# Kernel tuning notes

Measured on AMD Instinct MI355X. Metric: run time of the kernel, lower is better.

Reference implementation:

```python
import jax, jax.numpy as jnp
import numpy as np

FP8_MAX = 448.0  # e4m3 max, from scale = max(w) / (448.0 * 6.0) in the source


def setup_inputs() -> dict:
    key = jax.random.key(0)
    k_w, k_perm, k_x, k_b = jax.random.split(key, 4)
    T, K, O = 8192, 4096, 4096  # tokens = bsz*q_len, in_features, out_features

    # --- simulate init-time reorder_quantize_w ---
    w = jax.random.normal(k_w, (O, K), dtype=jnp.float32) * 0.02
    g_scale = jnp.max(jnp.abs(w)) / (FP8_MAX * 6.0)          # global weight scale
    perm = jax.random.permutation(k_perm, K)                  # outlier reorder index
    w_r = w[:, perm] / g_scale                                # reordered, globally scaled
    scale_w = jnp.max(jnp.abs(w_r), axis=1) / FP8_MAX         # per-out-channel scale (O,)
    W = jnp.round(w_r / scale_w[:, None])                     # quantized values (stored fp32)

    # --- simulate activation quantization (same reorder applied upstream) ---
    x = jax.random.normal(k_x, (T, K), dtype=jnp.float32)
    scale_x = (jnp.max(jnp.abs(x), axis=1, keepdims=True) / FP8_MAX)  # (T,1)
    qx = jnp.round(x / scale_x)                               # quantized values (stored fp32)

    bias = jax.random.normal(k_b, (O,), dtype=jnp.float32) * 0.01
    scale = jnp.asarray([g_scale], dtype=jnp.float32)         # fused global scale (x-global * w-global)

    return {"qx": qx, "W": W, "scale_x": scale_x, "scale_w": scale_w,
            "scale": scale, "bias": bias, "bsz": 4, "q_len": 2048}


def reference(qx, W, scale_x, scale_w, scale, bias, bsz, q_len):
    # agemm.matmul: low-bit GEMM with fused per-token (scale_x), per-channel (scale_w)
    # and global (scale) dequant scales.  y[t,o] = (sum_k qx[t,k]*W[o,k]) * sx[t] * sw[o] * s
    y = jnp.einsum('tk,ok->to', qx, W)           # (T, O) accumulate
    y = y * scale_x * scale_w[None, :] * scale[0]
    y = y + bias
    return y.reshape(bsz, q_len, -1)
```

## Files before the change

kernel.cpp:

```cpp
#include <hip/hip_runtime.h>

typedef __bf16 bf16_t;
typedef __bf16 bf16x8 __attribute__((ext_vector_type(8)));
typedef __bf16 bf16x4 __attribute__((ext_vector_type(4)));
typedef float f32x4 __attribute__((ext_vector_type(4)));

constexpr int TDIM = 8192;
constexpr int KDIM = 4096;
constexpr int ODIM = 4096;

__device__ __forceinline__ void async_ld16(void* lds, const void* g) {
    __builtin_amdgcn_global_load_lds(
        (const __attribute__((address_space(1))) unsigned int*)g,
        (__attribute__((address_space(3))) unsigned int*)lds,
        16, 0, 0);
}

__global__ __launch_bounds__(256) void cvt2_kernel(const float* __restrict__ a, bf16_t* __restrict__ da,
                                                   int nblk_a,
                                                   const float* __restrict__ w, bf16_t* __restrict__ dw) {
    int b = blockIdx.x;
    const float* src;
    bf16_t* dst;
    if (b < nblk_a) { src = a; dst = da; }
    else            { src = w; dst = dw; b -= nblk_a; }
    const size_t base = (size_t)b * 2048 + threadIdx.x * 8;
    const float4 v0 = *(const float4*)(src + base);
    const float4 v1 = *(const float4*)(src + base + 4);
    bf16x8 o;
    o[0] = (bf16_t)v0.x; o[1] = (bf16_t)v0.y; o[2] = (bf16_t)v0.z; o[3] = (bf16_t)v0.w;
    o[4] = (bf16_t)v1.x; o[5] = (bf16_t)v1.y; o[6] = (bf16_t)v1.z; o[7] = (bf16_t)v1.w;
    *(bf16x8*)(dst + base) = o;
}

constexpr int BM = 256, BN = 256, BK = 64;
constexpr int NKT = KDIM / BK;
constexpr int NIT = NKT / 2;

#define BAR   __builtin_amdgcn_s_barrier()
#define SCB   __builtin_amdgcn_sched_barrier(0)
#define WLG   asm volatile("s_waitcnt lgkmcnt(0)" ::: "memory")
#define WV6   asm volatile("s_waitcnt vmcnt(6)" ::: "memory")
#define WV0   asm volatile("s_waitcnt vmcnt(0)" ::: "memory")
#define PRIO1 __builtin_amdgcn_s_setprio(1)
#define PRIO0 __builtin_amdgcn_s_setprio(0)

#define STG_A(c, kt, h) \
    async_ld16(lds_a + (c)*32768 + (h)*16384,        a_srcb + (size_t)((h)*128     )*KDIM + (kt)*64); \
    async_ld16(lds_a + (c)*32768 + (h)*16384 + 8192, a_srcb + (size_t)((h)*128 + 64)*KDIM + (kt)*64)
#define STG_B(c, kt, h) \
    async_ld16(lds_b + (c)*32768 + (h)*16384,        b_srcb + (size_t)((h)*128     )*KDIM + (kt)*64); \
    async_ld16(lds_b + (c)*32768 + (h)*16384 + 8192, b_srcb + (size_t)((h)*128 + 64)*KDIM + (kt)*64)

#define LD_A_LO(c) _Pragma("unroll") for (int m = 0; m < 4; ++m) { \
    af[m][0] = *(const bf16x8*)(a_rd + (c)*32768 + m*2048 + ck0); \
    af[m][1] = *(const bf16x8*)(a_rd + (c)*32768 + m*2048 + ck1); }
#define LD_A_HI(c) _Pragma("unroll") for (int m = 0; m < 4; ++m) { \
    af[m][0] = *(const bf16x8*)(a_rd + (c)*32768 + (m+4)*2048 + ck0); \
    af[m][1] = *(const bf16x8*)(a_rd + (c)*32768 + (m+4)*2048 + ck1); }
#define LD_B01(c) _Pragma("unroll") for (int n = 0; n < 2; ++n) { \
    bfr[n][0] = *(const bf16x8*)(b_rd + (c)*32768 + n*2048 + ck0); \
    bfr[n][1] = *(const bf16x8*)(b_rd + (c)*32768 + n*2048 + ck1); }
#define LD_B23(c) _Pragma("unroll") for (int n = 2; n < 4; ++n) { \
    bfr[n][0] = *(const bf16x8*)(b_rd + (c)*32768 + n*2048 + ck0); \
    bfr[n][1] = *(const bf16x8*)(b_rd + (c)*32768 + n*2048 + ck1); }

#define MFMA16(MB, NB) \
  _Pragma("unroll") for (int m = 0; m < 4; ++m) \
  _Pragma("unroll") for (int n = 0; n < 2; ++n) \
  _Pragma("unroll") for (int k = 0; k < 2; ++k) \
    acc[(MB)+m][(NB)+n] = __builtin_amdgcn_mfma_f32_16x16x32_bf16( \
        af[m][k], bfr[(NB)+n][k], acc[(MB)+m][(NB)+n], 0, 0, 0)

__global__ __launch_bounds__(512, 2) void gemm8_kernel(
    const bf16_t* __restrict__ A, const bf16_t* __restrict__ B,
    const float* __restrict__ scale_x, const float* __restrict__ scale_w,
    const float* __restrict__ gscale, const float* __restrict__ bias,
    float* __restrict__ out)
{
    __shared__ __attribute__((aligned(16))) char smem[131072];

    const int tid = threadIdx.x;
    const int lin = (blockIdx.x & 7) * 64 + (blockIdx.x >> 3);
    const int row0 = (lin >> 4) * BM;
    const int col0 = (lin & 15) * BN;

    const int ld_row = tid >> 3;
    const int ld_ch  = (tid & 7) ^ (ld_row & 7);
    const bf16_t* a_srcb = A + (size_t)(row0 + ld_row) * KDIM + ld_ch * 8;
    const bf16_t* b_srcb = B + (size_t)(col0 + ld_row) * KDIM + ld_ch * 8;
    char* lds_a = smem + tid * 16;
    char* lds_b = smem + 65536 + tid * 16;

    const int lane = tid & 63;
    const int wid  = tid >> 6;
    const int wm   = wid >> 2;
    const int wn   = wid & 3;
    const int fr   = lane & 15;
    const int q    = lane >> 4;
    const int swz  = lane & 7;
    const int ck0  = ((q ^ swz)) * 16;
    const int ck1  = (((4 | q) ^ swz)) * 16;
    const char* a_rd = smem + (wm * 128 + fr) * 128;
    const char* b_rd = smem + 65536 + (wn * 64 + fr) * 128;

    f32x4 acc[8][4] = {};
    bf16x8 af[4][2], bfr[4][2];

    STG_B(0, 0, 0); STG_B(0, 0, 1);
    STG_A(0, 0, 0); STG_A(0, 0, 1);
    STG_B(1, 1, 0); STG_B(1, 1, 1);
    STG_A(1, 1, 0);
    WV6; SCB; BAR; SCB;
    LD_A_LO(0); LD_B01(0); SCB;

#pragma unroll 1
    for (int i = 0; i < NIT - 1; ++i) {
        const int tp = 2 * i + 2;
        STG_A(1, 2 * i + 1, 1);
        BAR; WLG; SCB;
        PRIO1; MFMA16(0, 0); PRIO0; SCB;
        LD_B23(0); SCB; BAR; SCB;
        STG_B(0, tp, 0);
        BAR; WLG; SCB;
        PRIO1; MFMA16(0, 2); PRIO0; SCB;
        LD_A_HI(0); SCB; BAR; SCB;
        STG_B(0, tp, 1);
        BAR; WLG; SCB;
        PRIO1; MFMA16(4, 0); PRIO0; SCB; BAR; SCB;
        STG_A(0, tp, 0);
        WV6; SCB; BAR; SCB;
        PRIO1; MFMA16(4, 2); PRIO0; SCB;
        LD_A_LO(1); LD_B01(1); SCB; BAR; SCB;
        STG_A(0, tp, 1);
        BAR; WLG; SCB;
        PRIO1; MFMA16(0, 0); PRIO0; SCB;
        LD_B23(1); SCB; BAR; SCB;
        STG_B(1, tp + 1, 0);
        BAR; WLG; SCB;
        PRIO1; MFMA16(0, 2); PRIO0; SCB;
        LD_A_HI(1); SCB; BAR; SCB;
        STG_B(1, tp + 1, 1);
        BAR; WLG; SCB;
        PRIO1; MFMA16(4, 0); PRIO0; SCB; BAR; SCB;
        STG_A(1, tp + 1, 0);
        WV6; SCB; BAR; SCB;
        PRIO1; MFMA16(4, 2); PRIO0; SCB;
        LD_A_LO(0); LD_B01(0);
        SCB; BAR; SCB;
    }

    {
        STG_A(1, NKT - 1, 1);
        BAR; WLG; SCB;
        PRIO1; MFMA16(0, 0); PRIO0; SCB;
        LD_B23(0); SCB; BAR; SCB;
        BAR; WLG; SCB;
        PRIO1; MFMA16(0, 2); PRIO0; SCB;
        LD_A_HI(0); SCB; BAR; SCB;
        BAR; WLG; SCB;
        PRIO1; MFMA16(4, 0); PRIO0; SCB; BAR; SCB;
        WV0; SCB; BAR; SCB;
        PRIO1; MFMA16(4, 2); PRIO0; SCB;
        LD_A_LO(1); LD_B01(1); SCB; BAR; SCB;
        BAR; WLG; SCB;
        PRIO1; MFMA16(0, 0); PRIO0; SCB;
        LD_B23(1); SCB; BAR; SCB;
        BAR; WLG; SCB;
        PRIO1; MFMA16(0, 2); PRIO0; SCB;
        LD_A_HI(1); SCB; BAR; SCB;
        BAR; WLG; SCB;
        PRIO1; MFMA16(4, 0); PRIO0; SCB; BAR; SCB;
        WV6; SCB; BAR; SCB;
        PRIO1; MFMA16(4, 2); PRIO0; SCB;
        SCB; BAR; SCB;
    }

    const float gs = gscale[0];
    const int trow = row0 + wm * 128 + q * 4;
    const int ocol = col0 + wn * 64 + fr;
#pragma unroll
    for (int nt = 0; nt < 4; ++nt) {
        const int o = ocol + nt * 16;
        const float sws = scale_w[o] * gs;
        const float bv = bias[o];
#pragma unroll
        for (int mt = 0; mt < 8; ++mt) {
#pragma unroll
            for (int ii = 0; ii < 4; ++ii) {
                const int t = trow + mt * 16 + ii;
                out[(size_t)t * ODIM + o] = acc[mt][nt][ii] * (scale_x[t] * sws) + bv;
            }
        }
    }
}

constexpr int FBM = 128, FBN = 128, FBK = 32;

__global__ __launch_bounds__(256, 4) void gemm_fallback(
    const float* __restrict__ Afp, const float* __restrict__ Bfp,
    const float* __restrict__ scale_x, const float* __restrict__ scale_w,
    const float* __restrict__ gscale, const float* __restrict__ bias,
    float* __restrict__ out) {
    __shared__ bf16_t sA[FBM * FBK];
    __shared__ bf16_t sB[FBN * FBK];

    const int tid = threadIdx.x;
    const int bn = blockIdx.x & 31;
    const int bm = blockIdx.x >> 5;
    const int row0 = bm * FBM;
    const int col0 = bn * FBN;

    const int lane = tid & 63;
    const int wid = tid >> 6;
    const int wm = (wid >> 1) * 64;
    const int wn = (wid & 1) * 64;
    const int fr = lane & 15;
    const int q  = lane >> 4;
    const int s_fr = (fr >> 1) & 3;
    const int kc = ((q ^ s_fr) * 8);

    f32x4 acc[4][4] = {};

    for (int k0 = 0; k0 < KDIM; k0 += FBK) {
        const int r = tid >> 2;
        const int cg2 = (tid & 3) ^ ((tid >> 3) & 3);
#pragma unroll
        for (int h = 0; h < 2; ++h) {
            const int rr = r + h * 64;
            const float4 va0 = *(const float4*)(Afp + (size_t)(row0 + rr) * KDIM + k0 + cg2 * 8);
            const float4 va1 = *(const float4*)(Afp + (size_t)(row0 + rr) * KDIM + k0 + cg2 * 8 + 4);
            const float4 vb0 = *(const float4*)(Bfp + (size_t)(col0 + rr) * KDIM + k0 + cg2 * 8);
            const float4 vb1 = *(const float4*)(Bfp + (size_t)(col0 + rr) * KDIM + k0 + cg2 * 8 + 4);
            bf16x8 pa, pb;
            pa[0] = (bf16_t)va0.x; pa[1] = (bf16_t)va0.y; pa[2] = (bf16_t)va0.z; pa[3] = (bf16_t)va0.w;
            pa[4] = (bf16_t)va1.x; pa[5] = (bf16_t)va1.y; pa[6] = (bf16_t)va1.z; pa[7] = (bf16_t)va1.w;
            pb[0] = (bf16_t)vb0.x; pb[1] = (bf16_t)vb0.y; pb[2] = (bf16_t)vb0.z; pb[3] = (bf16_t)vb0.w;
            pb[4] = (bf16_t)vb1.x; pb[5] = (bf16_t)vb1.y; pb[6] = (bf16_t)vb1.z; pb[7] = (bf16_t)vb1.w;
            *(bf16x8*)&sA[rr * FBK + (tid & 3) * 8] = pa;
            *(bf16x8*)&sB[rr * FBK + (tid & 3) * 8] = pb;
        }
        __syncthreads();

        bf16x8 a8[4], b8[4];
#pragma unroll
        for (int mt = 0; mt < 4; ++mt)
            a8[mt] = *(const bf16x8*)&sA[(wm + mt * 16 + fr) * FBK + kc];
#pragma unroll
        for (int nt = 0; nt < 4; ++nt)
            b8[nt] = *(const bf16x8*)&sB[(wn + nt * 16 + fr) * FBK + kc];
#pragma unroll
        for (int mt = 0; mt < 4; ++mt)
#pragma unroll
            for (int nt = 0; nt < 4; ++nt)
                acc[mt][nt] = __builtin_amdgcn_mfma_f32_16x16x32_bf16(a8[mt], b8[nt], acc[mt][nt], 0, 0, 0);
        __syncthreads();
    }

    const float gs = gscale[0];
    const int rbase = q * 4;
#pragma unroll
    for (int nt = 0; nt < 4; ++nt) {
        const int o = col0 + wn + nt * 16 + fr;
        const float swv = scale_w[o] * gs;
        const float bv = bias[o];
#pragma unroll
        for (int mt = 0; mt < 4; ++mt) {
#pragma unroll
            for (int i = 0; i < 4; ++i) {
                const int t = row0 + wm + mt * 16 + rbase + i;
                out[(size_t)t * ODIM + o] = acc[mt][nt][i] * (scale_x[t] * swv) + bv;
            }
        }
    }
}

extern "C" void kernel_launch(void* const* d_in, const int* in_sizes, int n_in,
                              void* d_out, int out_size, void* d_ws, size_t ws_size,
                              hipStream_t stream) {
    const float* qx   = (const float*)d_in[0];
    const float* W    = (const float*)d_in[1];
    const float* sx   = (const float*)d_in[2];
    const float* sw   = (const float*)d_in[3];
    const float* gs   = (const float*)d_in[4];
    const float* bias = (const float*)d_in[5];
    float* out = (float*)d_out;

    const size_t nA = (size_t)TDIM * KDIM;
    const size_t nW = (size_t)ODIM * KDIM;

    if (ws_size >= (nA + nW) * sizeof(bf16_t)) {
        bf16_t* Abf = (bf16_t*)d_ws;
        bf16_t* Wbf = Abf + nA;
        const int nblk_a = (int)(nA / 2048);
        const int nblk_w = (int)(nW / 2048);
        cvt2_kernel<<<dim3(nblk_a + nblk_w), dim3(256), 0, stream>>>(qx, Abf, nblk_a, W, Wbf);
        gemm8_kernel<<<dim3((TDIM / BM) * (ODIM / BN)), dim3(512), 0, stream>>>(
            Abf, Wbf, sx, sw, gs, bias, out);
    } else {
        gemm_fallback<<<dim3((TDIM / FBM) * (ODIM / FBN)), dim3(256), 0, stream>>>(
            qx, W, sx, sw, gs, bias, out);
    }
}
```

Measured before the change: 489.6 us.

## Double-buffer MFMA register fragments to spread LDS reads across sub-phases

```diff
diff --git a/kernel.cpp b/kernel.cpp
--- a/kernel.cpp
+++ b/kernel.cpp
@@ -41,6 +41,7 @@
 #define SCB   __builtin_amdgcn_sched_barrier(0)
 #define WLG   asm volatile("s_waitcnt lgkmcnt(0)" ::: "memory")
 #define WV6   asm volatile("s_waitcnt vmcnt(6)" ::: "memory")
+#define WV4   asm volatile("s_waitcnt vmcnt(4)" ::: "memory")
 #define WV0   asm volatile("s_waitcnt vmcnt(0)" ::: "memory")
 #define PRIO1 __builtin_amdgcn_s_setprio(1)
 #define PRIO0 __builtin_amdgcn_s_setprio(0)
@@ -52,25 +53,34 @@
     async_ld16(lds_b + (c)*32768 + (h)*16384,        b_srcb + (size_t)((h)*128     )*KDIM + (kt)*64); \
     async_ld16(lds_b + (c)*32768 + (h)*16384 + 8192, b_srcb + (size_t)((h)*128 + 64)*KDIM + (kt)*64)
 
-#define LD_A_LO(c) _Pragma("unroll") for (int m = 0; m < 4; ++m) { \
-    af[m][0] = *(const bf16x8*)(a_rd + (c)*32768 + m*2048 + ck0); \
-    af[m][1] = *(const bf16x8*)(a_rd + (c)*32768 + m*2048 + ck1); }
-#define LD_A_HI(c) _Pragma("unroll") for (int m = 0; m < 4; ++m) { \
-    af[m][0] = *(const bf16x8*)(a_rd + (c)*32768 + (m+4)*2048 + ck0); \
-    af[m][1] = *(const bf16x8*)(a_rd + (c)*32768 + (m+4)*2048 + ck1); }
-#define LD_B01(c) _Pragma("unroll") for (int n = 0; n < 2; ++n) { \
-    bfr[n][0] = *(const bf16x8*)(b_rd + (c)*32768 + n*2048 + ck0); \
-    bfr[n][1] = *(const bf16x8*)(b_rd + (c)*32768 + n*2048 + ck1); }
-#define LD_B23(c) _Pragma("unroll") for (int n = 2; n < 4; ++n) { \
-    bfr[n][0] = *(const bf16x8*)(b_rd + (c)*32768 + n*2048 + ck0); \
-    bfr[n][1] = *(const bf16x8*)(b_rd + (c)*32768 + n*2048 + ck1); }
-
-#define MFMA16(MB, NB) \
+#define RD_AFL(c) _Pragma("unroll") for (int m = 0; m < 4; ++m) { \
+    afL[m][0] = *(const bf16x8*)(a_rd + (c)*32768 + m*2048 + ck0); \
+    afL[m][1] = *(const bf16x8*)(a_rd + (c)*32768 + m*2048 + ck1); }
+#define RD_AFH_LO(c) _Pragma("unroll") for (int m = 0; m < 2; ++m) { \
+    afH[m][0] = *(const bf16x8*)(a_rd + (c)*32768 + (m+4)*2048 + ck0); \
+    afH[m][1] = *(const bf16x8*)(a_rd + (c)*32768 + (m+4)*2048 + ck1); }
+#define RD_AFH_HI(c) _Pragma("unroll") for (int m = 2; m < 4; ++m) { \
+    afH[m][0] = *(const bf16x8*)(a_rd + (c)*32768 + (m+4)*2048 + ck0); \
+    afH[m][1] = *(const bf16x8*)(a_rd + (c)*32768 + (m+4)*2048 + ck1); }
+#define RD_B01A(c) _Pragma("unroll") for (int n = 0; n < 2; ++n) { \
+    b01A[n][0] = *(const bf16x8*)(b_rd + (c)*32768 + n*2048 + ck0); \
+    b01A[n][1] = *(const bf16x8*)(b_rd + (c)*32768 + n*2048 + ck1); }
+#define RD_B23A(c) _Pragma("unroll") for (int n = 0; n < 2; ++n) { \
+    b23A[n][0] = *(const bf16x8*)(b_rd + (c)*32768 + (n+2)*2048 + ck0); \
+    b23A[n][1] = *(const bf16x8*)(b_rd + (c)*32768 + (n+2)*2048 + ck1); }
+#define RD_B01B(c) _Pragma("unroll") for (int n = 0; n < 2; ++n) { \
+    b01B[n][0] = *(const bf16x8*)(b_rd + (c)*32768 + n*2048 + ck0); \
+    b01B[n][1] = *(const bf16x8*)(b_rd + (c)*32768 + n*2048 + ck1); }
+#define RD_B23B(c) _Pragma("unroll") for (int n = 0; n < 2; ++n) { \
+    b23B[n][0] = *(const bf16x8*)(b_rd + (c)*32768 + (n+2)*2048 + ck0); \
+    b23B[n][1] = *(const bf16x8*)(b_rd + (c)*32768 + (n+2)*2048 + ck1); }
+
+#define MFMAQ(AF, MB, BF, NB) \
   _Pragma("unroll") for (int m = 0; m < 4; ++m) \
   _Pragma("unroll") for (int n = 0; n < 2; ++n) \
   _Pragma("unroll") for (int k = 0; k < 2; ++k) \
     acc[(MB)+m][(NB)+n] = __builtin_amdgcn_mfma_f32_16x16x32_bf16( \
-        af[m][k], bfr[(NB)+n][k], acc[(MB)+m][(NB)+n], 0, 0, 0)
+        AF[m][k], BF[n][k], acc[(MB)+m][(NB)+n], 0, 0, 0)
 
 __global__ __launch_bounds__(512, 2) void gemm8_kernel(
     const bf16_t* __restrict__ A, const bf16_t* __restrict__ B,
@@ -105,75 +115,77 @@
     const char* b_rd = smem + 65536 + (wn * 64 + fr) * 128;
 
     f32x4 acc[8][4] = {};
-    bf16x8 af[4][2], bfr[4][2];
+    bf16x8 afL[4][2], afH[4][2];
+    bf16x8 b01A[2][2], b23A[2][2], b01B[2][2], b23B[2][2];
 
     STG_B(0, 0, 0); STG_B(0, 0, 1);
     STG_A(0, 0, 0); STG_A(0, 0, 1);
     STG_B(1, 1, 0); STG_B(1, 1, 1);
     STG_A(1, 1, 0);
     WV6; SCB; BAR; SCB;
-    LD_A_LO(0); LD_B01(0); SCB;
+    RD_AFL(0); RD_B01A(0); RD_B23A(0); SCB;
 
 #pragma unroll 1
     for (int i = 0; i < NIT - 1; ++i) {
         const int tp = 2 * i + 2;
         STG_A(1, 2 * i + 1, 1);
         BAR; WLG; SCB;
-        PRIO1; MFMA16(0, 0); PRIO0; SCB;
-        LD_B23(0); SCB; BAR; SCB;
+        PRIO1; MFMAQ(afL, 0, b01A, 0); PRIO0; SCB;
+        RD_AFH_LO(0); SCB; BAR; SCB;
         STG_B(0, tp, 0);
-        BAR; WLG; SCB;
-        PRIO1; MFMA16(0, 2); PRIO0; SCB;
-        LD_A_HI(0); SCB; BAR; SCB;
+        WV6; SCB; BAR; SCB;
+        PRIO1; MFMAQ(afL, 0, b23A, 2); PRIO0; SCB;
+        RD_AFH_HI(0); RD_B01B(1); SCB; BAR; SCB;
         STG_B(0, tp, 1);
         BAR; WLG; SCB;
-        PRIO1; MFMA16(4, 0); PRIO0; SCB; BAR; SCB;
+        PRIO1; MFMAQ(afH, 4, b01A, 0); PRIO0; SCB;
+        RD_B23B(1); SCB; BAR; SCB;
         STG_A(0, tp, 0);
         WV6; SCB; BAR; SCB;
-        PRIO1; MFMA16(4, 2); PRIO0; SCB;
-        LD_A_LO(1); LD_B01(1); SCB; BAR; SCB;
+        PRIO1; MFMAQ(afH, 4, b23A, 2); PRIO0; SCB;
+        RD_AFL(1); SCB; BAR; SCB;
         STG_A(0, tp, 1);
         BAR; WLG; SCB;
-        PRIO1; MFMA16(0, 0); PRIO0; SCB;
-        LD_B23(1); SCB; BAR; SCB;
+        PRIO1; MFMAQ(afL, 0, b01B, 0); PRIO0; SCB;
+        RD_AFH_LO(1); SCB; BAR; SCB;
         STG_B(1, tp + 1, 0);
-        BAR; WLG; SCB;
-        PRIO1; MFMA16(0, 2); PRIO0; SCB;
-        LD_A_HI(1); SCB; BAR; SCB;
+        WV6; SCB; BAR; SCB;
+        PRIO1; MFMAQ(afL, 0, b23B, 2); PRIO0; SCB;
+        RD_AFH_HI(1); RD_B01A(0); SCB; BAR; SCB;
         STG_B(1, tp + 1, 1);
         BAR; WLG; SCB;
-        PRIO1; MFMA16(4, 0); PRIO0; SCB; BAR; SCB;
+        PRIO1; MFMAQ(afH, 4, b01B, 0); PRIO0; SCB;
+        RD_B23A(0); SCB; BAR; SCB;
         STG_A(1, tp + 1, 0);
         WV6; SCB; BAR; SCB;
-        PRIO1; MFMA16(4, 2); PRIO0; SCB;
-        LD_A_LO(0); LD_B01(0);
-        SCB; BAR; SCB;
+        PRIO1; MFMAQ(afH, 4, b23B, 2); PRIO0; SCB;
+        RD_AFL(0); SCB; BAR; SCB;
     }
 
     {
         STG_A(1, NKT - 1, 1);
         BAR; WLG; SCB;
-        PRIO1; MFMA16(0, 0); PRIO0; SCB;
-        LD_B23(0); SCB; BAR; SCB;
-        BAR; WLG; SCB;
-        PRIO1; MFMA16(0, 2); PRIO0; SCB;
-        LD_A_HI(0); SCB; BAR; SCB;
-        BAR; WLG; SCB;
-        PRIO1; MFMA16(4, 0); PRIO0; SCB; BAR; SCB;
+        PRIO1; MFMAQ(afL, 0, b01A, 0); PRIO0; SCB;
+        RD_AFH_LO(0); SCB; BAR; SCB;
+        WV4; SCB; BAR; SCB;
+        PRIO1; MFMAQ(afL, 0, b23A, 2); PRIO0; SCB;
+        RD_AFH_HI(0); RD_B01B(1); SCB; BAR; SCB;
+        BAR; WLG; SCB;
+        PRIO1; MFMAQ(afH, 4, b01A, 0); PRIO0; SCB;
+        RD_B23B(1); SCB; BAR; SCB;
         WV0; SCB; BAR; SCB;
-        PRIO1; MFMA16(4, 2); PRIO0; SCB;
-        LD_A_LO(1); LD_B01(1); SCB; BAR; SCB;
-        BAR; WLG; SCB;
-        PRIO1; MFMA16(0, 0); PRIO0; SCB;
-        LD_B23(1); SCB; BAR; SCB;
-        BAR; WLG; SCB;
-        PRIO1; MFMA16(0, 2); PRIO0; SCB;
-        LD_A_HI(1); SCB; BAR; SCB;
-        BAR; WLG; SCB;
-        PRIO1; MFMA16(4, 0); PRIO0; SCB; BAR; SCB;
-        WV6; SCB; BAR; SCB;
-        PRIO1; MFMA16(4, 2); PRIO0; SCB;
-        SCB; BAR; SCB;
+        PRIO1; MFMAQ(afH, 4, b23A, 2); PRIO0; SCB;
+        RD_AFL(1); SCB; BAR; SCB;
+        BAR; WLG; SCB;
+        PRIO1; MFMAQ(afL, 0, b01B, 0); PRIO0; SCB;
+        RD_AFH_LO(1); SCB; BAR; SCB;
+        BAR; SCB;
+        PRIO1; MFMAQ(afL, 0, b23B, 2); PRIO0; SCB;
+        RD_AFH_HI(1); SCB; BAR; SCB;
+        BAR; WLG; SCB;
+        PRIO1; MFMAQ(afH, 4, b01B, 0); PRIO0; SCB; BAR; SCB;
+        BAR; SCB;
+        PRIO1; MFMAQ(afH, 4, b23B, 2); PRIO0; SCB; BAR; SCB;
     }
 
     const float gs = gscale[0];
```

New measurement: 499.6 us. 1.02x slower.
